# Kernel optimization log

Hardware: AMD Instinct MI355X
Metric: run time of the kernel (lower is better)

Reference implementation:

```python
import jax, jax.numpy as jnp
import numpy as np

N_NODES = 100000
N_EDGES = 1600000
IN_DIM = 768
HIDDEN = 256
N_CLASSES = 3


def setup_inputs() -> dict:
    key = jax.random.key(0)
    k0, k1, k2, k3 = jax.random.split(key, 4)
    x = jax.random.normal(k0, (N_NODES, IN_DIM), dtype=jnp.float32)
    edge_index = jax.random.randint(k1, (2, N_EDGES), 0, N_NODES, dtype=jnp.int32)
    # Glorot-ish init for weights
    W1 = jax.random.normal(k2, (IN_DIM, HIDDEN), dtype=jnp.float32) * (1.0 / np.sqrt(IN_DIM))
    b1 = jnp.zeros((HIDDEN,), dtype=jnp.float32)
    W2 = jax.random.normal(k3, (HIDDEN, N_CLASSES), dtype=jnp.float32) * (1.0 / np.sqrt(HIDDEN))
    b2 = jnp.zeros((N_CLASSES,), dtype=jnp.float32)
    return {"x": x, "edge_index": edge_index, "W1": W1, "b1": b1, "W2": W2, "b2": b2}


def reference(x, edge_index, W1, b1, W2, b2):
    """dumb_GNN forward: GCNConv(768->H) -> relu -> (dropout=eval identity) -> Linear -> log_softmax.

    GCNConv math (PyG default): out = D^{-1/2} (A + I) D^{-1/2} X W + b
    """
    n = x.shape[0]
    src, dst = edge_index[0], edge_index[1]
    # add self-loops
    loops = jnp.arange(n, dtype=src.dtype)
    src = jnp.concatenate([src, loops])
    dst = jnp.concatenate([dst, loops])
    # symmetric degree normalization (degrees include self-loops)
    deg = jax.ops.segment_sum(jnp.ones_like(src, dtype=x.dtype), dst, num_segments=n)
    dinv = jnp.where(deg > 0, jax.lax.rsqrt(deg), jnp.zeros_like(deg))
    norm = dinv[src] * dinv[dst]  # [E+N]
    # transform then gather-scale-scatter aggregate
    h = x @ W1  # [N, H]
    agg = jax.ops.segment_sum(h[src] * norm[:, None], dst, num_segments=n) + b1
    h = jax.nn.relu(agg)
    # dropout is identity at inference
    logits = h @ W2 + b2  # [N, C]
    return jax.nn.log_softmax(logits, axis=-1)
```

## Files before the change

kernel.cpp:

```cpp
#include <hip/hip_runtime.h>
#include <hip/hip_bf16.h>
#include <math.h>

#define N_NODES 100000
#define N_EDGES 1600000
#define IN_DIM  768
#define HIDDEN  256

#define SCAN_B  256
#define N_SBLK  ((N_NODES + SCAN_B - 1) / SCAN_B)

#define H_OFF    0ull
#define ADJ_OFF  51200000ull
#define RS_OFF   57600000ull
#define CUR_OFF  58000016ull
#define DEG_OFF  58400016ull
#define DINV_OFF 58800016ull
#define W1T_OFF  59200016ull
#define BSUM_OFF 59593232ull

typedef short          bf16x8 __attribute__((ext_vector_type(8)));
typedef float          fp32x4 __attribute__((ext_vector_type(4)));
typedef unsigned short u16x4  __attribute__((ext_vector_type(4)));

__device__ inline short f2bf(float f) {
    union { float f; unsigned u; } c; c.f = f;
    unsigned u = c.u;
    unsigned r = u + 0x7FFFu + ((u >> 16) & 1u);
    return (short)(r >> 16);
}

__device__ inline fp32x4 bf4_to_f4(u16x4 v) {
    fp32x4 r;
    for (int j = 0; j < 4; j++) {
        union { unsigned u; float f; } c;
        c.u = ((unsigned)v[j]) << 16;
        r[j] = c.f;
    }
    return r;
}

__device__ inline void async16(const void* g, void* l) {
    __builtin_amdgcn_global_load_lds(
        (const __attribute__((address_space(1))) unsigned int*)g,
        (__attribute__((address_space(3))) unsigned int*)l,
        16, 0, 0);
}

__global__ void init_kernel(int* __restrict__ deg, int* __restrict__ cursor) {
    int i = blockIdx.x * blockDim.x + threadIdx.x;
    if (i < N_NODES) { deg[i] = 0; cursor[i] = 0; }
}

__global__ void w1t_kernel(const float* __restrict__ w1, short* __restrict__ w1t) {
    int i = blockIdx.x * blockDim.x + threadIdx.x;
    if (i < HIDDEN * IN_DIM) {
        int n = i / IN_DIM, k = i % IN_DIM;
        w1t[i] = f2bf(w1[(size_t)k * HIDDEN + n]);
    }
}

__global__ void count_kernel(const int* __restrict__ dst, int* __restrict__ deg) {
    int e = blockIdx.x * blockDim.x + threadIdx.x;
    if (e < N_EDGES) atomicAdd(&deg[dst[e]], 1);
}

__global__ __launch_bounds__(SCAN_B) void scan1_kernel(const int* __restrict__ deg,
                                                       int* __restrict__ bsum) {
    int i = blockIdx.x * SCAN_B + threadIdx.x;
    int v = (i < N_NODES) ? deg[i] : 0;
    for (int off = 32; off > 0; off >>= 1) v += __shfl_down(v, off, 64);
    __shared__ int wsum[SCAN_B / 64];
    int lane = threadIdx.x & 63, w = threadIdx.x >> 6;
    if (lane == 0) wsum[w] = v;
    __syncthreads();
    if (threadIdx.x == 0) {
        int s = 0;
        for (int j = 0; j < SCAN_B / 64; j++) s += wsum[j];
        bsum[blockIdx.x] = s;
    }
}

__global__ __launch_bounds__(512) void scan2_kernel(int* __restrict__ bsum) {
    __shared__ int s[512];
    int tid = threadIdx.x;
    int v = (tid < N_SBLK) ? bsum[tid] : 0;
    s[tid] = v;
    __syncthreads();
    for (int off = 1; off < 512; off <<= 1) {
        int t = (tid >= off) ? s[tid - off] : 0;
        __syncthreads();
        s[tid] += t;
        __syncthreads();
    }
    if (tid < N_SBLK) bsum[tid] = s[tid] - v;
}

__global__ __launch_bounds__(SCAN_B) void scan3_kernel(const int* __restrict__ deg,
                                                       const int* __restrict__ bsum,
                                                       int* __restrict__ row_start,
                                                       float* __restrict__ dinv) {
    __shared__ int s[SCAN_B];
    int i = blockIdx.x * SCAN_B + threadIdx.x;
    int tid = threadIdx.x;
    int d = (i < N_NODES) ? deg[i] : 0;
    s[tid] = d;
    __syncthreads();
    for (int off = 1; off < SCAN_B; off <<= 1) {
        int t = (tid >= off) ? s[tid - off] : 0;
        __syncthreads();
        s[tid] += t;
        __syncthreads();
    }
    if (i < N_NODES) {
        row_start[i] = bsum[blockIdx.x] + s[tid] - d;
        dinv[i] = rsqrtf((float)(d + 1));
        if (i == N_NODES - 1) row_start[N_NODES] = N_EDGES;
    }
}

__global__ void fill_kernel(const int* __restrict__ src, const int* __restrict__ dst,
                            const int* __restrict__ row_start, int* __restrict__ cursor,
                            int* __restrict__ adj) {
    int e = blockIdx.x * blockDim.x + threadIdx.x;
    if (e < N_EDGES) {
        int d = dst[e];
        int p = row_start[d] + atomicAdd(&cursor[d], 1);
        adj[p] = src[e];
    }
}

__global__ __launch_bounds__(256) void gemm1_kernel(const float* __restrict__ x,
                                                    const short* __restrict__ w1t,
                                                    const float* __restrict__ dinv,
                                                    unsigned short* __restrict__ h) {
    __shared__ float a_lds[2][128 * 32];
    __shared__ short b_lds[2][128 * 32];

    const int tid  = threadIdx.x;
    const int lane = tid & 63;
    const int wave = tid >> 6;
    const int wm = (wave >> 1) * 64;
    const int wn = (wave & 1) * 64;
    const int l15 = lane & 15;
    const int q   = lane >> 4;
    const int row0 = blockIdx.x * 128;
    const int col0 = blockIdx.y * 128;

    const float* ag[4];
    int alo[4];
#pragma unroll
    for (int i = 0; i < 4; i++) {
        int cd = (wave * 4 + i) * 64 + lane;
        int ar = cd >> 3;
        int asrc = (cd & 7) ^ (ar & 7);
        int grow = row0 + ar;
        if (grow >= N_NODES) grow = N_NODES - 1;
        ag[i]  = x + (size_t)grow * IN_DIM + asrc * 4;
        alo[i] = cd * 16;
    }
    const short* bg[2];
    int blo[2];
#pragma unroll
    for (int i = 0; i < 2; i++) {
        int cd = (wave * 2 + i) * 64 + lane;
        int br = cd >> 2;
        int bsrc = (cd & 3) ^ ((br >> 1) & 3);
        bg[i]  = w1t + (size_t)(col0 + br) * IN_DIM + bsrc * 8;
        blo[i] = cd * 16;
    }

    fp32x4 acc[4][4];
#pragma unroll
    for (int i = 0; i < 4; i++)
#pragma unroll
        for (int j = 0; j < 4; j++)
#pragma unroll
            for (int r = 0; r < 4; r++) acc[i][j][r] = 0.0f;

#define STAGE(buf, k0) do {                                                   \
        char* ab = (char*)a_lds[buf];                                         \
        char* bb = (char*)b_lds[buf];                                         \
        async16(ag[0] + (k0), ab + alo[0]);                                   \
        async16(ag[1] + (k0), ab + alo[1]);                                   \
        async16(ag[2] + (k0), ab + alo[2]);                                   \
        async16(ag[3] + (k0), ab + alo[3]);                                   \
        async16(bg[0] + (k0), bb + blo[0]);                                   \
        async16(bg[1] + (k0), bb + blo[1]);                                   \
    } while (0)

    STAGE(0, 0);
    __syncthreads();

    int cur = 0;
    for (int k0 = 0; k0 < IN_DIM; k0 += 32) {
        int kn = k0 + 32;
        if (kn < IN_DIM) STAGE(cur ^ 1, kn);

        bf16x8 af[4], bfr[4];
#pragma unroll
        for (int mt = 0; mt < 4; mt++) {
            int ar = wm + mt * 16 + l15;
            const float* ap = &a_lds[cur][ar * 32];
            int c0 = (2 * q) ^ (ar & 7);
            fp32x4 f0 = *(const fp32x4*)(ap + (c0 << 2));
            fp32x4 f1 = *(const fp32x4*)(ap + ((c0 ^ 1) << 2));
            bf16x8 av;
            av[0] = f2bf(f0[0]); av[1] = f2bf(f0[1]);
            av[2] = f2bf(f0[2]); av[3] = f2bf(f0[3]);
            av[4] = f2bf(f1[0]); av[5] = f2bf(f1[1]);
            av[6] = f2bf(f1[2]); av[7] = f2bf(f1[3]);
            af[mt] = av;
        }
#pragma unroll
        for (int nt = 0; nt < 4; nt++) {
            int br = wn + nt * 16 + l15;
            int bs = q ^ ((br >> 1) & 3);
            bfr[nt] = *(const bf16x8*)(&b_lds[cur][br * 32 + bs * 8]);
        }
#pragma unroll
        for (int mt = 0; mt < 4; mt++)
#pragma unroll
            for (int nt = 0; nt < 4; nt++)
                acc[mt][nt] = __builtin_amdgcn_mfma_f32_16x16x32_bf16(
                    af[mt], bfr[nt], acc[mt][nt], 0, 0, 0);

        __syncthreads();
        cur ^= 1;
    }
#undef STAGE

    float dv[4][4];
#pragma unroll
    for (int mt = 0; mt < 4; mt++)
#pragma unroll
        for (int r = 0; r < 4; r++) {
            int row = row0 + wm + mt * 16 + q * 4 + r;
            dv[mt][r] = (row < N_NODES) ? dinv[row] : 0.0f;
        }
#pragma unroll
    for (int mt = 0; mt < 4; mt++) {
#pragma unroll
        for (int nt = 0; nt < 4; nt++) {
            int col = col0 + wn + nt * 16 + l15;
#pragma unroll
            for (int r = 0; r < 4; r++) {
                int row = row0 + wm + mt * 16 + q * 4 + r;
                if (row < N_NODES)
                    h[(size_t)row * HIDDEN + col] =
                        (unsigned short)f2bf(dv[mt][r] * acc[mt][nt][r]);
            }
        }
    }
}

__global__ __launch_bounds__(256) void aggregate_kernel(
    const unsigned short* __restrict__ h, const int* __restrict__ adj,
    const int* __restrict__ row_start, const float* __restrict__ dinv,
    const float* __restrict__ b1, const float* __restrict__ w2,
    const float* __restrict__ b2, float* __restrict__ out) {
    const int lane = threadIdx.x & 63;
    const int wave = threadIdx.x >> 6;
    const int v = blockIdx.x * 4 + wave;
    if (v >= N_NODES) return;

    const size_t loff = (size_t)lane * 4;

    fp32x4 a0 = bf4_to_f4(*(const u16x4*)(h + (size_t)v * HIDDEN + loff));
    fp32x4 a1 = {0,0,0,0}, a2 = {0,0,0,0}, a3 = {0,0,0,0};

    int e0 = row_start[v], e1 = row_start[v + 1];
    for (int e = e0; e < e1; e += 64) {
        int cnt = min(64, e1 - e);
        int s = (lane < cnt) ? adj[e + lane] : 0;
        int i = 0;
        for (; i + 4 <= cnt; i += 4) {
            int s0 = __shfl(s, i,     64);
            int s1 = __shfl(s, i + 1, 64);
            int s2 = __shfl(s, i + 2, 64);
            int s3 = __shfl(s, i + 3, 64);
            u16x4 r0 = *(const u16x4*)(h + (size_t)s0 * HIDDEN + loff);
            u16x4 r1 = *(const u16x4*)(h + (size_t)s1 * HIDDEN + loff);
            u16x4 r2 = *(const u16x4*)(h + (size_t)s2 * HIDDEN + loff);
            u16x4 r3 = *(const u16x4*)(h + (size_t)s3 * HIDDEN + loff);
            a0 += bf4_to_f4(r0);
            a1 += bf4_to_f4(r1);
            a2 += bf4_to_f4(r2);
            a3 += bf4_to_f4(r3);
        }
        for (; i < cnt; i++) {
            int si = __shfl(s, i, 64);
            a0 += bf4_to_f4(*(const u16x4*)(h + (size_t)si * HIDDEN + loff));
        }
    }
    fp32x4 acc = (a0 + a1) + (a2 + a3);

    float dvv = dinv[v];
    fp32x4 bb = *(const fp32x4*)(b1 + loff);
    float hr[4];
    for (int j = 0; j < 4; j++) hr[j] = fmaxf(0.0f, dvv * acc[j] + bb[j]);

    float p0 = 0.f, p1 = 0.f, p2 = 0.f;
    for (int j = 0; j < 4; j++) {
        const float* wr = w2 + (size_t)(lane * 4 + j) * 3;
        p0 += hr[j] * wr[0];
        p1 += hr[j] * wr[1];
        p2 += hr[j] * wr[2];
    }
    for (int off = 32; off > 0; off >>= 1) {
        p0 += __shfl_down(p0, off, 64);
        p1 += __shfl_down(p1, off, 64);
        p2 += __shfl_down(p2, off, 64);
    }
    if (lane == 0) {
        p0 += b2[0]; p1 += b2[1]; p2 += b2[2];
        float m = fmaxf(p0, fmaxf(p1, p2));
        float l = logf(expf(p0 - m) + expf(p1 - m) + expf(p2 - m));
        out[(size_t)v * 3 + 0] = p0 - m - l;
        out[(size_t)v * 3 + 1] = p1 - m - l;
        out[(size_t)v * 3 + 2] = p2 - m - l;
    }
}

extern "C" void kernel_launch(void* const* d_in, const int* in_sizes, int n_in,
                              void* d_out, int out_size, void* d_ws, size_t ws_size,
                              hipStream_t stream) {
    const float* x    = (const float*)d_in[0];
    const int*   ei   = (const int*)d_in[1];
    const float* W1   = (const float*)d_in[2];
    const float* b1   = (const float*)d_in[3];
    const float* W2   = (const float*)d_in[4];
    const float* b2   = (const float*)d_in[5];
    float* out = (float*)d_out;

    const int* src = ei;
    const int* dst = ei + N_EDGES;

    char* ws = (char*)d_ws;
    unsigned short* h_ws = (unsigned short*)(ws + H_OFF);
    int*   adj       = (int*)(ws + ADJ_OFF);
    int*   row_start = (int*)(ws + RS_OFF);
    int*   cursor    = (int*)(ws + CUR_OFF);
    int*   deg       = (int*)(ws + DEG_OFF);
    float* dinv      = (float*)(ws + DINV_OFF);
    short* w1t       = (short*)(ws + W1T_OFF);
    int*   bsum      = (int*)(ws + BSUM_OFF);

    init_kernel<<<(N_NODES + 255) / 256, 256, 0, stream>>>(deg, cursor);
    w1t_kernel<<<(HIDDEN * IN_DIM + 255) / 256, 256, 0, stream>>>(W1, w1t);
    count_kernel<<<(N_EDGES + 255) / 256, 256, 0, stream>>>(dst, deg);
    scan1_kernel<<<N_SBLK, SCAN_B, 0, stream>>>(deg, bsum);
    scan2_kernel<<<1, 512, 0, stream>>>(bsum);
    scan3_kernel<<<N_SBLK, SCAN_B, 0, stream>>>(deg, bsum, row_start, dinv);
    fill_kernel<<<(N_EDGES + 255) / 256, 256, 0, stream>>>(src, dst, row_start, cursor, adj);
    gemm1_kernel<<<dim3((N_NODES + 127) / 128, HIDDEN / 128), 256, 0, stream>>>(x, w1t, dinv, h_ws);
    aggregate_kernel<<<N_NODES / 4, 256, 0, stream>>>(h_ws, adj, row_start, dinv, b1, W2, b2, out);
}
```

Baseline: 783.6 us.

## Convert A tile to bf16 once in registers and remap workgroups across XCDs

The fp32 A tile of the first GEMM is no longer copied asynchronously into LDS and converted on every fragment read. Each thread now loads it into registers, converts it to bf16 once, and writes it into a swizzled bf16 LDS buffer after the MFMAs, so the global load overlaps compute. This halves A's LDS footprint and removes the redundant per-wave conversions. The grid becomes 1D with an XCD-aware block remap so that both column halves of a row tile land on the same XCD and share L2. In exchange, the A loads are now synchronous register loads and register pressure goes up.

```diff
diff --git a/kernel.cpp b/kernel.cpp
--- a/kernel.cpp
+++ b/kernel.cpp
@@ -134,8 +134,8 @@
                                                     const short* __restrict__ w1t,
                                                     const float* __restrict__ dinv,
                                                     unsigned short* __restrict__ h) {
-    __shared__ float a_lds[2][128 * 32];
-    __shared__ short b_lds[2][128 * 32];
+    __shared__ __align__(16) short a_lds[2 * 128 * 32];
+    __shared__ __align__(16) short b_lds[2 * 128 * 32];
 
     const int tid  = threadIdx.x;
     const int lane = tid & 63;
@@ -144,29 +144,32 @@
     const int wn = (wave & 1) * 64;
     const int l15 = lane & 15;
     const int q   = lane >> 4;
-    const int row0 = blockIdx.x * 128;
-    const int col0 = blockIdx.y * 128;
-
-    const float* ag[4];
-    int alo[4];
-#pragma unroll
-    for (int i = 0; i < 4; i++) {
-        int cd = (wave * 4 + i) * 64 + lane;
-        int ar = cd >> 3;
-        int asrc = (cd & 7) ^ (ar & 7);
-        int grow = row0 + ar;
-        if (grow >= N_NODES) grow = N_NODES - 1;
-        ag[i]  = x + (size_t)grow * IN_DIM + asrc * 4;
-        alo[i] = cd * 16;
-    }
+
+    const int nwg = gridDim.x;
+    const int xq = nwg >> 3, xr = nwg & 7;
+    const int orig = blockIdx.x;
+    const int xcd = orig & 7, idx = orig >> 3;
+    const int wgid = (xcd < xr ? xcd * (xq + 1) : xr * (xq + 1) + (xcd - xr) * xq) + idx;
+    const int row0 = (wgid >> 1) * 128;
+    const int col0 = (wgid & 1) * 128;
+
+    const int ar = tid >> 1;
+    const int kh = tid & 1;
+    int garow = row0 + ar;
+    if (garow >= N_NODES) garow = N_NODES - 1;
+    const float* axp = x + (size_t)garow * IN_DIM + kh * 16;
+    const int asw  = (ar >> 1) & 3;
+    const int aoff0 = ar * 32 + (((kh * 2 + 0) ^ asw) << 3);
+    const int aoff1 = ar * 32 + (((kh * 2 + 1) ^ asw) << 3);
+
     const short* bg[2];
     int blo[2];
 #pragma unroll
     for (int i = 0; i < 2; i++) {
         int cd = (wave * 2 + i) * 64 + lane;
         int br = cd >> 2;
-        int bsrc = (cd & 3) ^ ((br >> 1) & 3);
-        bg[i]  = w1t + (size_t)(col0 + br) * IN_DIM + bsrc * 8;
+        int c  = cd & 3;
+        bg[i]  = w1t + (size_t)(col0 + br) * IN_DIM + ((c ^ ((br >> 1) & 3)) * 8);
         blo[i] = cd * 16;
     }
 
@@ -178,46 +181,61 @@
 #pragma unroll
             for (int r = 0; r < 4; r++) acc[i][j][r] = 0.0f;
 
-#define STAGE(buf, k0) do {                                                   \
-        char* ab = (char*)a_lds[buf];                                         \
-        char* bb = (char*)b_lds[buf];                                         \
-        async16(ag[0] + (k0), ab + alo[0]);                                   \
-        async16(ag[1] + (k0), ab + alo[1]);                                   \
-        async16(ag[2] + (k0), ab + alo[2]);                                   \
-        async16(ag[3] + (k0), ab + alo[3]);                                   \
+#define BSTAGE(buf, k0) do {                                                  \
+        char* bb = (char*)(b_lds + (buf) * (128 * 32));                       \
         async16(bg[0] + (k0), bb + blo[0]);                                   \
         async16(bg[1] + (k0), bb + blo[1]);                                   \
     } while (0)
 
-    STAGE(0, 0);
-    __syncthreads();
+#define AWRITE(buf, v0, v1, v2, v3) do {                                      \
+        short* ad = a_lds + (buf) * (128 * 32);                               \
+        bf16x8 wv;                                                            \
+        wv[0] = f2bf(v0[0]); wv[1] = f2bf(v0[1]);                             \
+        wv[2] = f2bf(v0[2]); wv[3] = f2bf(v0[3]);                             \
+        wv[4] = f2bf(v1[0]); wv[5] = f2bf(v1[1]);                             \
+        wv[6] = f2bf(v1[2]); wv[7] = f2bf(v1[3]);                             \
+        *(bf16x8*)(ad + aoff0) = wv;                                          \
+        wv[0] = f2bf(v2[0]); wv[1] = f2bf(v2[1]);                             \
+        wv[2] = f2bf(v2[2]); wv[3] = f2bf(v2[3]);                             \
+        wv[4] = f2bf(v3[0]); wv[5] = f2bf(v3[1]);                             \
+        wv[6] = f2bf(v3[2]); wv[7] = f2bf(v3[3]);                             \
+        *(bf16x8*)(ad + aoff1) = wv;                                          \
+    } while (0)
+
+    {
+        fp32x4 na0 = *(const fp32x4*)(axp + 0);
+        fp32x4 na1 = *(const fp32x4*)(axp + 4);
+        fp32x4 na2 = *(const fp32x4*)(axp + 8);
+        fp32x4 na3 = *(const fp32x4*)(axp + 12);
+        BSTAGE(0, 0);
+        AWRITE(0, na0, na1, na2, na3);
+        __syncthreads();
+    }
+
+    const int fsw = q ^ ((l15 >> 1) & 3);
 
     int cur = 0;
-    for (int k0 = 0; k0 < IN_DIM; k0 += 32) {
-        int kn = k0 + 32;
-        if (kn < IN_DIM) STAGE(cur ^ 1, kn);
-
+    for (int t = 0; t < IN_DIM / 32; ++t) {
+        const int kn = (t + 1) * 32;
+        const bool more = kn < IN_DIM;
+        fp32x4 na0, na1, na2, na3;
+        if (more) {
+            na0 = *(const fp32x4*)(axp + kn);
+            na1 = *(const fp32x4*)(axp + kn + 4);
+            na2 = *(const fp32x4*)(axp + kn + 8);
+            na3 = *(const fp32x4*)(axp + kn + 12);
+            BSTAGE(cur ^ 1, kn);
+        }
+
+        const short* ac = a_lds + cur * (128 * 32);
+        const short* bc = b_lds + cur * (128 * 32);
         bf16x8 af[4], bfr[4];
 #pragma unroll
-        for (int mt = 0; mt < 4; mt++) {
-            int ar = wm + mt * 16 + l15;
-            const float* ap = &a_lds[cur][ar * 32];
-            int c0 = (2 * q) ^ (ar & 7);
-            fp32x4 f0 = *(const fp32x4*)(ap + (c0 << 2));
-            fp32x4 f1 = *(const fp32x4*)(ap + ((c0 ^ 1) << 2));
-            bf16x8 av;
-            av[0] = f2bf(f0[0]); av[1] = f2bf(f0[1]);
-            av[2] = f2bf(f0[2]); av[3] = f2bf(f0[3]);
-            av[4] = f2bf(f1[0]); av[5] = f2bf(f1[1]);
-            av[6] = f2bf(f1[2]); av[7] = f2bf(f1[3]);
-            af[mt] = av;
-        }
-#pragma unroll
-        for (int nt = 0; nt < 4; nt++) {
-            int br = wn + nt * 16 + l15;
-            int bs = q ^ ((br >> 1) & 3);
-            bfr[nt] = *(const bf16x8*)(&b_lds[cur][br * 32 + bs * 8]);
-        }
+        for (int mt = 0; mt < 4; mt++)
+            af[mt] = *(const bf16x8*)(ac + (wm + mt * 16 + l15) * 32 + (fsw << 3));
+#pragma unroll
+        for (int nt = 0; nt < 4; nt++)
+            bfr[nt] = *(const bf16x8*)(bc + (wn + nt * 16 + l15) * 32 + (fsw << 3));
 #pragma unroll
         for (int mt = 0; mt < 4; mt++)
 #pragma unroll
@@ -225,10 +243,13 @@
                 acc[mt][nt] = __builtin_amdgcn_mfma_f32_16x16x32_bf16(
                     af[mt], bfr[nt], acc[mt][nt], 0, 0, 0);
 
+        if (more) AWRITE(cur ^ 1, na0, na1, na2, na3);
+
         __syncthreads();
         cur ^= 1;
     }
-#undef STAGE
+#undef BSTAGE
+#undef AWRITE
 
     float dv[4][4];
 #pragma unroll
@@ -353,6 +374,6 @@
     scan2_kernel<<<1, 512, 0, stream>>>(bsum);
     scan3_kernel<<<N_SBLK, SCAN_B, 0, stream>>>(deg, bsum, row_start, dinv);
     fill_kernel<<<(N_EDGES + 255) / 256, 256, 0, stream>>>(src, dst, row_start, cursor, adj);
-    gemm1_kernel<<<dim3((N_NODES + 127) / 128, HIDDEN / 128), 256, 0, stream>>>(x, w1t, dinv, h_ws);
+    gemm1_kernel<<<(N_NODES + 127) / 128 * 2, 256, 0, stream>>>(x, w1t, dinv, h_ws);
     aggregate_kernel<<<N_NODES / 4, 256, 0, stream>>>(h_ws, adj, row_start, dinv, b1, W2, b2, out);
 }
```

Result: faster. 753.5 us (-3.8%).
